# Performance work log

Measured on AMD Instinct MI355X. Metric: run time of the kernel, lower is better.

Reference implementation:

```python
import jax, jax.numpy as jnp
import numpy as np


def setup_inputs() -> dict:
    key = jax.random.key(0)
    k1, k2, k3 = jax.random.split(key, 3)
    B, Lx, Ly, D = 8, 2048, 2048, 512  # D = 2*hidden_size
    x = jax.random.normal(k1, (B, Lx, D), dtype=jnp.float32)
    y = jax.random.normal(k2, (B, Ly, D), dtype=jnp.float32)
    # torch nn.Linear weight: [out_features, in_features], applied as x @ W.T
    Wb = jax.random.normal(k3, (D, D), dtype=jnp.float32) * (1.0 / np.sqrt(D))
    return {"x": x, "y": y, "Wb": Wb}


def reference(x, y, Wb):
    # _s1 = Wb(x).transpose(2,1): project x then transpose -> scores s_jt = y @ (x Wb^T)^T
    xw = jnp.einsum('bxd,ed->bxe', x, Wb)          # [B, Lx, D], equals x @ Wb.T
    sjt = jnp.einsum('byd,bxd->byx', y, xw)        # [B, Ly, Lx]
    ait = jax.nn.softmax(sjt, axis=-1)             # softmax over Lx
    qtb = jnp.einsum('byx,bxd->byd', ait, x)       # [B, Ly, D]
    return qtb
```

## Files before the change

### kernel.cpp

```cpp
#include <hip/hip_runtime.h>
#include <hip/hip_bf16.h>
#include <math.h>

#define D_DIM 512
#define LX 2048
#define LY 2048
#define NB 8

typedef float f32x4 __attribute__((ext_vector_type(4)));
typedef __bf16 bf16x8 __attribute__((ext_vector_type(8)));

__device__ __forceinline__ unsigned short f2bf_rn(float f) {
    unsigned u = __float_as_uint(f);
    unsigned r = (u + 0x7fffu + ((u >> 16) & 1u)) >> 16;
    return (unsigned short)r;
}
__device__ __forceinline__ float bf2f(unsigned short h) {
    return __uint_as_float(((unsigned)h) << 16);
}
__device__ __forceinline__ void async16(void* lds, const void* g) {
    __builtin_amdgcn_global_load_lds(
        (const __attribute__((address_space(1))) void*)g,
        (__attribute__((address_space(3))) void*)lds, 16, 0, 0);
}
__device__ __forceinline__ bf16x8 ldfrag(const char* p) {
    return *(const bf16x8*)p;
}

__global__ __launch_bounds__(256) void repack_hilo_k(
    const float* __restrict__ src, unsigned short* __restrict__ dh,
    unsigned short* __restrict__ dl, int nfb)
{
    int fbid = blockIdx.x * 4 + (threadIdx.x >> 6);
    if (fbid >= nfb) return;
    int lane = threadIdx.x & 63;
    int r16 = fbid >> 4, k32 = fbid & 15;
    int row = r16 * 16 + (lane & 15);
    int col = k32 * 32 + (lane >> 4) * 8;
    const float* s = src + (size_t)row * D_DIM + col;
    float4 v0 = *(const float4*)s;
    float4 v1 = *(const float4*)(s + 4);
    float vv[8] = {v0.x, v0.y, v0.z, v0.w, v1.x, v1.y, v1.z, v1.w};
    unsigned hh[4], ll[4];
    #pragma unroll
    for (int k = 0; k < 4; ++k) {
        unsigned short ha = f2bf_rn(vv[2*k]),   hb = f2bf_rn(vv[2*k+1]);
        unsigned short la = f2bf_rn(vv[2*k]   - bf2f(ha));
        unsigned short lb = f2bf_rn(vv[2*k+1] - bf2f(hb));
        hh[k] = (unsigned)ha | ((unsigned)hb << 16);
        ll[k] = (unsigned)la | ((unsigned)lb << 16);
    }
    size_t off = (size_t)fbid * 512 + lane * 8;
    *(uint4*)(dh + off) = make_uint4(hh[0], hh[1], hh[2], hh[3]);
    *(uint4*)(dl + off) = make_uint4(ll[0], ll[1], ll[2], ll[3]);
}

__global__ __launch_bounds__(256) void xt_repack_k(
    const float* __restrict__ x, unsigned short* __restrict__ xtf)
{
    __shared__ unsigned short T2[64][72];
    int ct = blockIdx.x, dt = blockIdx.y, b = blockIdx.z;
    int tid = threadIdx.x;
    const float* xb = x + (size_t)b * LX * D_DIM;
    int rc = tid >> 4;
    int d4 = (tid & 15) * 4;
    #pragma unroll
    for (int i = 0; i < 4; ++i) {
        int cl = rc + i * 16;
        float4 v = *(const float4*)(xb + (size_t)(ct * 64 + cl) * D_DIM + dt * 64 + d4);
        T2[d4 + 0][cl] = f2bf_rn(v.x);
        T2[d4 + 1][cl] = f2bf_rn(v.y);
        T2[d4 + 2][cl] = f2bf_rn(v.z);
        T2[d4 + 3][cl] = f2bf_rn(v.w);
    }
    __syncthreads();
    #pragma unroll
    for (int si = 0; si < 2; ++si) {
        int s = tid + si * 256;
        int fb = s >> 6, lane = s & 63;
        int dd16l = fb >> 1, c32l = fb & 1;
        int ddl = dd16l * 16 + (lane & 15);
        int cl  = c32l * 32 + (lane >> 4) * 8;
        uint4 v = *(const uint4*)&T2[ddl][cl];
        size_t off = ((size_t)((b * 32 + dt * 4 + dd16l) * 64 + (ct * 2 + c32l)) * 64 + lane) * 8;
        *(uint4*)(xtf + off) = v;
    }
}

__global__ __launch_bounds__(256, 2) void xw_mfma_k(
    const unsigned short* __restrict__ xfh, const unsigned short* __restrict__ xfl,
    const unsigned short* __restrict__ wfh, const unsigned short* __restrict__ wfl,
    unsigned short* __restrict__ xwfh, unsigned short* __restrict__ xwfl)
{
    __shared__ char smem[49152];
    const int tid = threadIdx.x, lane = tid & 63, w = tid >> 6;
    const int Mt = blockIdx.x, Nt = blockIdx.y;
    f32x4 acc[2][4];
    #pragma unroll
    for (int m = 0; m < 2; ++m)
        #pragma unroll
        for (int n = 0; n < 4; ++n) acc[m][n] = (f32x4){0.f, 0.f, 0.f, 0.f};

    for (int kc = 0; kc < 8; ++kc) {
        __syncthreads();
        #pragma unroll
        for (int i = 0; i < 8; ++i) {
            int seg = w + 4 * i;
            int h = seg >> 4, c16l = (seg >> 1) & 7, k32l = seg & 1;
            size_t fb = (size_t)(Mt * 8 + c16l) * 16 + kc * 2 + k32l;
            const unsigned short* src = (h ? xfl : xfh) + fb * 512 + lane * 8;
            char* dst = smem + (h ? 16384 : 0) + ((c16l * 2 + k32l) * 64 + lane) * 16;
            async16(dst, src);
        }
        #pragma unroll
        for (int i = 0; i < 4; ++i) {
            int seg = w + 4 * i;
            int h = seg >> 3, n16l = (seg >> 1) & 3, k32l = seg & 1;
            size_t fb = (size_t)(Nt * 4 + n16l) * 16 + kc * 2 + k32l;
            const unsigned short* src = (h ? wfl : wfh) + fb * 512 + lane * 8;
            char* dst = smem + (h ? 40960 : 32768) + ((n16l * 2 + k32l) * 64 + lane) * 16;
            async16(dst, src);
        }
        __syncthreads();
        #pragma unroll
        for (int ks = 0; ks < 2; ++ks) {
            bf16x8 ah[2], al[2], bh[4], bl[4];
            #pragma unroll
            for (int m = 0; m < 2; ++m) {
                int c16l = w * 2 + m;
                ah[m] = ldfrag(smem +     0 + ((c16l * 2 + ks) * 64 + lane) * 16);
                al[m] = ldfrag(smem + 16384 + ((c16l * 2 + ks) * 64 + lane) * 16);
            }
            #pragma unroll
            for (int n = 0; n < 4; ++n) {
                bh[n] = ldfrag(smem + 32768 + ((n * 2 + ks) * 64 + lane) * 16);
                bl[n] = ldfrag(smem + 40960 + ((n * 2 + ks) * 64 + lane) * 16);
            }
            #pragma unroll
            for (int m = 0; m < 2; ++m)
                #pragma unroll
                for (int n = 0; n < 4; ++n) {
                    acc[m][n] = __builtin_amdgcn_mfma_f32_16x16x32_bf16(ah[m], bh[n], acc[m][n], 0, 0, 0);
                    acc[m][n] = __builtin_amdgcn_mfma_f32_16x16x32_bf16(ah[m], bl[n], acc[m][n], 0, 0, 0);
                    acc[m][n] = __builtin_amdgcn_mfma_f32_16x16x32_bf16(al[m], bh[n], acc[m][n], 0, 0, 0);
                    acc[m][n] = __builtin_amdgcn_mfma_f32_16x16x32_bf16(al[m], bl[n], acc[m][n], 0, 0, 0);
                }
        }
    }
    __syncthreads();
    float* E = (float*)smem;
    const int q = lane >> 4, c15 = lane & 15;
    #pragma unroll
    for (int m = 0; m < 2; ++m)
        #pragma unroll
        for (int n = 0; n < 4; ++n)
            #pragma unroll
            for (int r = 0; r < 4; ++r)
                E[(w * 32 + m * 16 + q * 4 + r) * 68 + n * 16 + c15] = acc[m][n][r];
    __syncthreads();
    #pragma unroll
    for (int i = 0; i < 4; ++i) {
        int s = tid + i * 256;
        int c16l = s >> 7, e32l = (s >> 6) & 1, lp = s & 63;
        int row = c16l * 16 + (lp & 15), col = e32l * 32 + (lp >> 4) * 8;
        const float* sp = E + row * 68 + col;
        unsigned hh[4], ll[4];
        #pragma unroll
        for (int k = 0; k < 4; ++k) {
            float a = sp[2 * k], bq = sp[2 * k + 1];
            unsigned short ha = f2bf_rn(a), hb = f2bf_rn(bq);
            unsigned short la = f2bf_rn(a - bf2f(ha)), lb = f2bf_rn(bq - bf2f(hb));
            hh[k] = (unsigned)ha | ((unsigned)hb << 16);
            ll[k] = (unsigned)la | ((unsigned)lb << 16);
        }
        size_t fb = (size_t)(Mt * 8 + c16l) * 16 + (Nt * 2 + e32l);
        *(uint4*)(xwfh + fb * 512 + lp * 8) = make_uint4(hh[0], hh[1], hh[2], hh[3]);
        *(uint4*)(xwfl + fb * 512 + lp * 8) = make_uint4(ll[0], ll[1], ll[2], ll[3]);
    }
}

__global__ __launch_bounds__(256, 2) void flash_mfma_k(
    const unsigned short* __restrict__ yfh, const unsigned short* __restrict__ yfl,
    const unsigned short* __restrict__ xwfh, const unsigned short* __restrict__ xwfl,
    const unsigned short* __restrict__ xtf, float* __restrict__ out)
{
    __shared__ char smem[49152];
    const int tid = threadIdx.x, lane = tid & 63, w = tid >> 6;
    const int jt = blockIdx.x, b = blockIdx.y;
    const int q = lane >> 4, c15 = lane & 15;

    f32x4 o[2][8];
    #pragma unroll
    for (int m = 0; m < 2; ++m)
        #pragma unroll
        for (int n = 0; n < 8; ++n) o[m][n] = (f32x4){0.f, 0.f, 0.f, 0.f};
    float m_run[2][4], l_run[2][4];
    #pragma unroll
    for (int m = 0; m < 2; ++m)
        #pragma unroll
        for (int r = 0; r < 4; ++r) { m_run[m][r] = -INFINITY; l_run[m][r] = 0.f; }

    for (int xt = 0; xt < 16; ++xt) {
        f32x4 s[2][2];
        #pragma unroll
        for (int m = 0; m < 2; ++m)
            #pragma unroll
            for (int n = 0; n < 2; ++n) s[m][n] = (f32x4){0.f, 0.f, 0.f, 0.f};

        for (int kc = 0; kc < 8; ++kc) {
            __syncthreads();
            #pragma unroll
            for (int i = 0; i < 8; ++i) {
                int seg = w + 4 * i;
                int h = seg >> 4, c16l = (seg >> 1) & 7, k32l = seg & 1;
                size_t fb = (size_t)(b * 128 + xt * 8 + c16l) * 16 + kc * 2 + k32l;
                const unsigned short* src = (h ? xwfl : xwfh) + fb * 512 + lane * 8;
                char* dst = smem + (h ? 16384 : 0) + ((c16l * 2 + k32l) * 64 + lane) * 16;
                async16(dst, src);
            }
            #pragma unroll
            for (int i = 0; i < 2; ++i) {
                int seg = w + 4 * i;
                int h = seg >> 2, j16l = (seg >> 1) & 1, k32l = seg & 1;
                size_t fb = (size_t)(b * 128 + jt * 2 + j16l) * 16 + kc * 2 + k32l;
                const unsigned short* src = (h ? yfl : yfh) + fb * 512 + lane * 8;
                char* dst = smem + (h ? 36864 : 32768) + ((j16l * 2 + k32l) * 64 + lane) * 16;
                async16(dst, src);
            }
            __syncthreads();
            #pragma unroll
            for (int ks = 0; ks < 2; ++ks) {
                bf16x8 ah[2], al[2], bh[2], bl[2];
                #pragma unroll
                for (int m = 0; m < 2; ++m) {
                    ah[m] = ldfrag(smem + 32768 + ((m * 2 + ks) * 64 + lane) * 16);
                    al[m] = ldfrag(smem + 36864 + ((m * 2 + ks) * 64 + lane) * 16);
                }
                #pragma unroll
                for (int n = 0; n < 2; ++n) {
                    int c16l = w * 2 + n;
                    bh[n] = ldfrag(smem +     0 + ((c16l * 2 + ks) * 64 + lane) * 16);
                    bl[n] = ldfrag(smem + 16384 + ((c16l * 2 + ks) * 64 + lane) * 16);
                }
                #pragma unroll
                for (int m = 0; m < 2; ++m)
                    #pragma unroll
                    for (int n = 0; n < 2; ++n) {
                        s[m][n] = __builtin_amdgcn_mfma_f32_16x16x32_bf16(ah[m], bh[n], s[m][n], 0, 0, 0);
                        s[m][n] = __builtin_amdgcn_mfma_f32_16x16x32_bf16(ah[m], bl[n], s[m][n], 0, 0, 0);
                        s[m][n] = __builtin_amdgcn_mfma_f32_16x16x32_bf16(al[m], bh[n], s[m][n], 0, 0, 0);
                        s[m][n] = __builtin_amdgcn_mfma_f32_16x16x32_bf16(al[m], bl[n], s[m][n], 0, 0, 0);
                    }
            }
        }

        float pmax[2][4];
        #pragma unroll
        for (int m = 0; m < 2; ++m)
            #pragma unroll
            for (int r = 0; r < 4; ++r) pmax[m][r] = fmaxf(s[m][0][r], s[m][1][r]);
        __syncthreads();
        #pragma unroll
        for (int d = 1; d < 16; d <<= 1)
            #pragma unroll
            for (int m = 0; m < 2; ++m)
                #pragma unroll
                for (int r = 0; r < 4; ++r)
                    pmax[m][r] = fmaxf(pmax[m][r], __shfl_xor(pmax[m][r], d, 64));
        float* red_max = (float*)(smem + 32768);
        float* red_sum = (float*)(smem + 33280);
        if (c15 == 0) {
            #pragma unroll
            for (int m = 0; m < 2; ++m)
                #pragma unroll
                for (int r = 0; r < 4; ++r)
                    red_max[w * 32 + m * 16 + q * 4 + r] = pmax[m][r];
        }
        __syncthreads();
        float mnew[2][4], alpha[2][4];
        #pragma unroll
        for (int m = 0; m < 2; ++m)
            #pragma unroll
            for (int r = 0; r < 4; ++r) {
                int j = m * 16 + q * 4 + r;
                float t = red_max[j];
                t = fmaxf(t, red_max[32 + j]);
                t = fmaxf(t, red_max[64 + j]);
                t = fmaxf(t, red_max[96 + j]);
                float mn = fmaxf(m_run[m][r], t);
                mnew[m][r] = mn;
                alpha[m][r] = __expf(m_run[m][r] - mn);
                m_run[m][r] = mn;
            }
        unsigned short* Pf = (unsigned short*)(smem + 40960);
        float psum[2][4];
        #pragma unroll
        for (int m = 0; m < 2; ++m)
            #pragma unroll
            for (int r = 0; r < 4; ++r) {
                float p0 = __expf(s[m][0][r] - mnew[m][r]);
                float p1 = __expf(s[m][1][r] - mnew[m][r]);
                s[m][0][r] = p0; s[m][1][r] = p1;
                psum[m][r] = p0 + p1;
            }
        #pragma unroll
        for (int d = 1; d < 16; d <<= 1)
            #pragma unroll
            for (int m = 0; m < 2; ++m)
                #pragma unroll
                for (int r = 0; r < 4; ++r)
                    psum[m][r] += __shfl_xor(psum[m][r], d, 64);
        if (c15 == 0) {
            #pragma unroll
            for (int m = 0; m < 2; ++m)
                #pragma unroll
                for (int r = 0; r < 4; ++r)
                    red_sum[w * 32 + m * 16 + q * 4 + r] = psum[m][r];
        }
        #pragma unroll
        for (int m = 0; m < 2; ++m)
            #pragma unroll
            for (int n = 0; n < 2; ++n)
                #pragma unroll
                for (int r = 0; r < 4; ++r) {
                    int cl = n * 16 + c15;
                    int lp = (q * 4 + r) + 16 * (cl >> 3);
                    Pf[((m * 4 + w) * 64 + lp) * 8 + (cl & 7)] = f2bf_rn(s[m][n][r]);
                }
        __syncthreads();
        #pragma unroll
        for (int m = 0; m < 2; ++m)
            #pragma unroll
            for (int r = 0; r < 4; ++r) {
                int j = m * 16 + q * 4 + r;
                float ts = red_sum[j] + red_sum[32 + j] + red_sum[64 + j] + red_sum[96 + j];
                l_run[m][r] = l_run[m][r] * alpha[m][r] + ts;
            }
        #pragma unroll
        for (int m = 0; m < 2; ++m)
            #pragma unroll
            for (int n = 0; n < 8; ++n)
                #pragma unroll
                for (int r = 0; r < 4; ++r) o[m][n][r] *= alpha[m][r];

        for (int cc = 0; cc < 4; ++cc) {
            #pragma unroll
            for (int i = 0; i < 8; ++i) {
                int dd16 = w + 4 * i;
                size_t off = ((size_t)(b * 32 + dd16) * 64 + (xt * 4 + cc)) * 512 + lane * 8;
                async16(smem + dd16 * 1024 + lane * 16, xtf + off);
            }
            __syncthreads();
            bf16x8 pa[2];
            pa[0] = ldfrag(smem + 40960 + ((0 * 4 + cc) * 64 + lane) * 16);
            pa[1] = ldfrag(smem + 40960 + ((1 * 4 + cc) * 64 + lane) * 16);
            #pragma unroll
            for (int n = 0; n < 8; ++n) {
                bf16x8 xb = ldfrag(smem + (w * 8 + n) * 1024 + lane * 16);
                o[0][n] = __builtin_amdgcn_mfma_f32_16x16x32_bf16(pa[0], xb, o[0][n], 0, 0, 0);
                o[1][n] = __builtin_amdgcn_mfma_f32_16x16x32_bf16(pa[1], xb, o[1][n], 0, 0, 0);
            }
            __syncthreads();
        }
    }

    #pragma unroll
    for (int m = 0; m < 2; ++m)
        #pragma unroll
        for (int r = 0; r < 4; ++r) {
            float inv = 1.0f / l_run[m][r];
            int j = jt * 32 + m * 16 + q * 4 + r;
            #pragma unroll
            for (int n = 0; n < 8; ++n) {
                int dd = w * 128 + n * 16 + c15;
                out[((size_t)(b * 2048 + j)) * 512 + dd] = o[m][n][r] * inv;
            }
        }
}

__global__ __launch_bounds__(256) void xw_gemm_fb(
    const float* __restrict__ x, const float* __restrict__ Wb, float* __restrict__ xw)
{
    __shared__ float As[16][68];
    __shared__ float Bs[16][68];
    const int tid = threadIdx.x;
    const int bm = blockIdx.x * 64, bn = blockIdx.y * 64;
    const int tm = (tid & 15) * 4, tn = (tid >> 4) * 4;
    const int lrow = tid >> 2, lk = (tid & 3) * 4;
    const float* ag = x  + (size_t)(bm + lrow) * D_DIM + lk;
    const float* bg = Wb + (size_t)(bn + lrow) * D_DIM + lk;
    float acc[4][4] = {};
    for (int kt = 0; kt < D_DIM; kt += 16) {
        const float4 av = *(const float4*)(ag + kt);
        const float4 bv = *(const float4*)(bg + kt);
        __syncthreads();
        As[lk+0][lrow] = av.x; As[lk+1][lrow] = av.y; As[lk+2][lrow] = av.z; As[lk+3][lrow] = av.w;
        Bs[lk+0][lrow] = bv.x; Bs[lk+1][lrow] = bv.y; Bs[lk+2][lrow] = bv.z; Bs[lk+3][lrow] = bv.w;
        __syncthreads();
        #pragma unroll
        for (int k = 0; k < 16; ++k) {
            const float4 a = *(const float4*)&As[k][tm];
            const float4 bq = *(const float4*)&Bs[k][tn];
            const float* ap = (const float*)&a;
            const float* bp = (const float*)&bq;
            #pragma unroll
            for (int i = 0; i < 4; ++i)
                #pragma unroll
                for (int jj = 0; jj < 4; ++jj)
                    acc[i][jj] = fmaf(ap[i], bp[jj], acc[i][jj]);
        }
    }
    #pragma unroll
    for (int i = 0; i < 4; ++i)
        *(float4*)&xw[(size_t)(bm + tm + i) * D_DIM + bn + tn] =
            make_float4(acc[i][0], acc[i][1], acc[i][2], acc[i][3]);
}

__global__ __launch_bounds__(256) void flash_fb(
    const float* __restrict__ x, const float* __restrict__ y,
    const float* __restrict__ xw, float* __restrict__ out)
{
    __shared__ float Yl[16][516];
    __shared__ float XWl[64][68];
    __shared__ float Pl[16][68];
    __shared__ float Xl[8][512];
    const int tid = threadIdx.x, b = blockIdx.y, jtb = blockIdx.x;
    const int j = tid >> 4, tc = tid & 15, c0 = tc * 4;
    {
        const float* yg = y + (size_t)(b * LY + jtb * 16 + j) * D_DIM;
        #pragma unroll
// ... 42 lines not shown
        const float p0 = __expf(sa[0] - mnew), p1 = __expf(sa[1] - mnew);
        const float p2 = __expf(sa[2] - mnew), p3 = __expf(sa[3] - mnew);
        float ts = p0 + p1 + p2 + p3;
        #pragma unroll
        for (int ww = 1; ww < 16; ww <<= 1) ts += __shfl_xor(ts, ww, 64);
        l = l * scale + ts; m = mnew;
        #pragma unroll
        for (int ii = 0; ii < 8; ++ii) {
            o[ii].x *= scale; o[ii].y *= scale; o[ii].z *= scale; o[ii].w *= scale;
        }
        *(float4*)&Pl[j][c0] = make_float4(p0, p1, p2, p3);
        for (int ccc = 0; ccc < 8; ++ccc) {
            const int xr = tid >> 5, xq = (tid & 31) * 4;
            const float* xg = x + xbase + (size_t)(xtt * 64 + ccc * 8 + xr) * D_DIM + xq;
            const float4 x0 = *(const float4*)(xg + 0);
            const float4 x1 = *(const float4*)(xg + 128);
            const float4 x2 = *(const float4*)(xg + 256);
            const float4 x3 = *(const float4*)(xg + 384);
            __syncthreads();
            *(float4*)&Xl[xr][xq +   0] = x0; *(float4*)&Xl[xr][xq + 128] = x1;
            *(float4*)&Xl[xr][xq + 256] = x2; *(float4*)&Xl[xr][xq + 384] = x3;
            __syncthreads();
            #pragma unroll
            for (int c = 0; c < 8; ++c) {
                const float pv = Pl[j][ccc * 8 + c];
                #pragma unroll
                for (int ii = 0; ii < 8; ++ii) {
                    const float4 xv = *(const float4*)&Xl[c][tc * 4 + 64 * ii];
                    o[ii].x = fmaf(pv, xv.x, o[ii].x); o[ii].y = fmaf(pv, xv.y, o[ii].y);
                    o[ii].z = fmaf(pv, xv.z, o[ii].z); o[ii].w = fmaf(pv, xv.w, o[ii].w);
                }
            }
        }
    }
    const float inv = 1.0f / l;
    float* og = out + (size_t)(b * LY + jtb * 16 + j) * D_DIM;
    #pragma unroll
    for (int ii = 0; ii < 8; ++ii) {
        float4 v = o[ii];
        v.x *= inv; v.y *= inv; v.z *= inv; v.w *= inv;
        *(float4*)(og + tc * 4 + 64 * ii) = v;
    }
}

extern "C" void kernel_launch(void* const* d_in, const int* in_sizes, int n_in,
                              void* d_out, int out_size, void* d_ws, size_t ws_size,
                              hipStream_t stream)
{
    const float* x  = (const float*)d_in[0];
    const float* y  = (const float*)d_in[1];
    const float* Wb = (const float*)d_in[2];
    float* out = (float*)d_out;

    const size_t SZ_BIG = 16777216;
    const size_t OFF_XFH = 0,         OFF_XFL = 16777216;
    const size_t OFF_YFH = 33554432,  OFF_YFL = 50331648;
    const size_t OFF_XTF = 67108864;
    const size_t OFF_XWH = 83886080,  OFF_XWL = 100663296;
    const size_t OFF_WFH = 117440512, OFF_WFL = 117964800;
    const size_t NEEDED = 118489088;
    (void)SZ_BIG;

    if (ws_size >= NEEDED) {
        char* ws = (char*)d_ws;
        unsigned short* xfh = (unsigned short*)(ws + OFF_XFH);
        unsigned short* xfl = (unsigned short*)(ws + OFF_XFL);
        unsigned short* yfh = (unsigned short*)(ws + OFF_YFH);
        unsigned short* yfl = (unsigned short*)(ws + OFF_YFL);
        unsigned short* xtf = (unsigned short*)(ws + OFF_XTF);
        unsigned short* xwfh = (unsigned short*)(ws + OFF_XWH);
        unsigned short* xwfl = (unsigned short*)(ws + OFF_XWL);
        unsigned short* wfh = (unsigned short*)(ws + OFF_WFH);
        unsigned short* wfl = (unsigned short*)(ws + OFF_WFL);

        repack_hilo_k<<<4096, 256, 0, stream>>>(x, xfh, xfl, 16384);
        repack_hilo_k<<<4096, 256, 0, stream>>>(y, yfh, yfl, 16384);
        repack_hilo_k<<<128, 256, 0, stream>>>(Wb, wfh, wfl, 512);
        dim3 gt(32, 8, 8);
        xt_repack_k<<<gt, 256, 0, stream>>>(x, xtf);
        dim3 g1(128, 8);
        xw_mfma_k<<<g1, 256, 0, stream>>>(xfh, xfl, wfh, wfl, xwfh, xwfl);
        dim3 g2(64, 8);
        flash_mfma_k<<<g2, 256, 0, stream>>>(yfh, yfl, xwfh, xwfl, xtf, out);
    } else {
        float* xw = (float*)d_ws;
        dim3 g1(NB * LX / 64, D_DIM / 64);
        xw_gemm_fb<<<g1, 256, 0, stream>>>(x, Wb, xw);
        dim3 g2(LY / 16, NB);
        flash_fb<<<g2, 256, 0, stream>>>(x, y, xw, out);
    }
}
```

Before: 395.7 us.

## Split flash attention over Lx into two partitions with a combine pass, drop lo*lo MFMA

The flash kernel is split along the Lx dimension into two halves (grid z adds a split index), each writing fp16 partial outputs plus running max/sum, and a new combine kernel merges them in fp32. This doubles the block count (64x8 to 64x2x8) for better CU occupancy, and the launch bound is raised to 3 blocks per CU. The score tile is widened to 64 x-columns per wave with a different K-chunking. The lo*lo bf16 split-precision MFMA term is dropped in both the xW GEMM and the score GEMM, which cuts MFMA work but slightly reduces accuracy. The fp16 partials and the extra combine pass add memory traffic and some precision loss.

```diff
diff --git a/kernel.cpp b/kernel.cpp
--- a/kernel.cpp
+++ b/kernel.cpp
@@ -1,5 +1,6 @@
 #include <hip/hip_runtime.h>
 #include <hip/hip_bf16.h>
+#include <hip/hip_fp16.h>
 #include <math.h>
 
 #define D_DIM 512
@@ -143,7 +144,6 @@
                     acc[m][n] = __builtin_amdgcn_mfma_f32_16x16x32_bf16(ah[m], bh[n], acc[m][n], 0, 0, 0);
                     acc[m][n] = __builtin_amdgcn_mfma_f32_16x16x32_bf16(ah[m], bl[n], acc[m][n], 0, 0, 0);
                     acc[m][n] = __builtin_amdgcn_mfma_f32_16x16x32_bf16(al[m], bh[n], acc[m][n], 0, 0, 0);
-                    acc[m][n] = __builtin_amdgcn_mfma_f32_16x16x32_bf16(al[m], bl[n], acc[m][n], 0, 0, 0);
                 }
         }
     }
@@ -179,15 +179,19 @@
     }
 }
 
-__global__ __launch_bounds__(256, 2) void flash_mfma_k(
+__global__ __launch_bounds__(256, 3) void flash2_k(
     const unsigned short* __restrict__ yfh, const unsigned short* __restrict__ yfl,
     const unsigned short* __restrict__ xwfh, const unsigned short* __restrict__ xwfl,
-    const unsigned short* __restrict__ xtf, float* __restrict__ out)
-{
-    __shared__ char smem[49152];
+    const unsigned short* __restrict__ xtf,
+    __half* __restrict__ part, float* __restrict__ mpart, float* __restrict__ lpart)
+{
+    __shared__ char smem[46080];
     const int tid = threadIdx.x, lane = tid & 63, w = tid >> 6;
-    const int jt = blockIdx.x, b = blockIdx.y;
+    const int jt = blockIdx.x, sp = blockIdx.y, b = blockIdx.z;
     const int q = lane >> 4, c15 = lane & 15;
+    unsigned short* Pf = (unsigned short*)(smem + 36864);
+    float* red_max = (float*)(smem + 45056);
+    float* red_sum = (float*)(smem + 45568);
 
     f32x4 o[2][8];
     #pragma unroll
@@ -200,57 +204,46 @@
         #pragma unroll
         for (int r = 0; r < 4; ++r) { m_run[m][r] = -INFINITY; l_run[m][r] = 0.f; }
 
-    for (int xt = 0; xt < 16; ++xt) {
-        f32x4 s[2][2];
+    for (int xt = 0; xt < 4; ++xt) {
+        f32x4 sa[2][4];
         #pragma unroll
         for (int m = 0; m < 2; ++m)
             #pragma unroll
-            for (int n = 0; n < 2; ++n) s[m][n] = (f32x4){0.f, 0.f, 0.f, 0.f};
-
-        for (int kc = 0; kc < 8; ++kc) {
+            for (int n = 0; n < 4; ++n) sa[m][n] = (f32x4){0.f, 0.f, 0.f, 0.f};
+
+        for (int kc = 0; kc < 16; ++kc) {
             __syncthreads();
             #pragma unroll
             for (int i = 0; i < 8; ++i) {
                 int seg = w + 4 * i;
-                int h = seg >> 4, c16l = (seg >> 1) & 7, k32l = seg & 1;
-                size_t fb = (size_t)(b * 128 + xt * 8 + c16l) * 16 + kc * 2 + k32l;
+                int h = seg >> 4, c16l = seg & 15;
+                size_t fb = ((size_t)(b * 128 + sp * 64 + xt * 16 + c16l)) * 16 + kc;
                 const unsigned short* src = (h ? xwfl : xwfh) + fb * 512 + lane * 8;
-                char* dst = smem + (h ? 16384 : 0) + ((c16l * 2 + k32l) * 64 + lane) * 16;
-                async16(dst, src);
-            }
-            #pragma unroll
-            for (int i = 0; i < 2; ++i) {
-                int seg = w + 4 * i;
-                int h = seg >> 2, j16l = (seg >> 1) & 1, k32l = seg & 1;
-                size_t fb = (size_t)(b * 128 + jt * 2 + j16l) * 16 + kc * 2 + k32l;
+                async16(smem + h * 16384 + (c16l * 64 + lane) * 16, src);
+            }
+            {
+                int h = w >> 1, j16l = w & 1;
+                size_t fb = ((size_t)(b * 128 + jt * 2 + j16l)) * 16 + kc;
                 const unsigned short* src = (h ? yfl : yfh) + fb * 512 + lane * 8;
-                char* dst = smem + (h ? 36864 : 32768) + ((j16l * 2 + k32l) * 64 + lane) * 16;
-                async16(dst, src);
+                async16(smem + 32768 + h * 2048 + j16l * 1024 + lane * 16, src);
             }
             __syncthreads();
-            #pragma unroll
-            for (int ks = 0; ks < 2; ++ks) {
-                bf16x8 ah[2], al[2], bh[2], bl[2];
+            bf16x8 ah[2], al[2];
+            ah[0] = ldfrag(smem + 32768 + lane * 16);
+            ah[1] = ldfrag(smem + 32768 + 1024 + lane * 16);
+            al[0] = ldfrag(smem + 34816 + lane * 16);
+            al[1] = ldfrag(smem + 34816 + 1024 + lane * 16);
+            #pragma unroll
+            for (int n = 0; n < 4; ++n) {
+                int c16l = w * 4 + n;
+                bf16x8 bh = ldfrag(smem + (c16l * 64 + lane) * 16);
+                bf16x8 bl = ldfrag(smem + 16384 + (c16l * 64 + lane) * 16);
                 #pragma unroll
                 for (int m = 0; m < 2; ++m) {
-                    ah[m] = ldfrag(smem + 32768 + ((m * 2 + ks) * 64 + lane) * 16);
-                    al[m] = ldfrag(smem + 36864 + ((m * 2 + ks) * 64 + lane) * 16);
-                }
-                #pragma unroll
-                for (int n = 0; n < 2; ++n) {
-                    int c16l = w * 2 + n;
-                    bh[n] = ldfrag(smem +     0 + ((c16l * 2 + ks) * 64 + lane) * 16);
-                    bl[n] = ldfrag(smem + 16384 + ((c16l * 2 + ks) * 64 + lane) * 16);
-                }
-                #pragma unroll
-                for (int m = 0; m < 2; ++m)
-                    #pragma unroll
-                    for (int n = 0; n < 2; ++n) {
-                        s[m][n] = __builtin_amdgcn_mfma_f32_16x16x32_bf16(ah[m], bh[n], s[m][n], 0, 0, 0);
-                        s[m][n] = __builtin_amdgcn_mfma_f32_16x16x32_bf16(ah[m], bl[n], s[m][n], 0, 0, 0);
-                        s[m][n] = __builtin_amdgcn_mfma_f32_16x16x32_bf16(al[m], bh[n], s[m][n], 0, 0, 0);
-                        s[m][n] = __builtin_amdgcn_mfma_f32_16x16x32_bf16(al[m], bl[n], s[m][n], 0, 0, 0);
-                    }
+                    sa[m][n] = __builtin_amdgcn_mfma_f32_16x16x32_bf16(ah[m], bh, sa[m][n], 0, 0, 0);
+                    sa[m][n] = __builtin_amdgcn_mfma_f32_16x16x32_bf16(ah[m], bl, sa[m][n], 0, 0, 0);
+                    sa[m][n] = __builtin_amdgcn_mfma_f32_16x16x32_bf16(al[m], bh, sa[m][n], 0, 0, 0);
+                }
             }
         }
 
@@ -258,8 +251,9 @@
         #pragma unroll
         for (int m = 0; m < 2; ++m)
             #pragma unroll
-            for (int r = 0; r < 4; ++r) pmax[m][r] = fmaxf(s[m][0][r], s[m][1][r]);
-        __syncthreads();
+            for (int r = 0; r < 4; ++r)
+                pmax[m][r] = fmaxf(fmaxf(sa[m][0][r], sa[m][1][r]),
+                                   fmaxf(sa[m][2][r], sa[m][3][r]));
         #pragma unroll
         for (int d = 1; d < 16; d <<= 1)
             #pragma unroll
@@ -267,8 +261,6 @@
                 #pragma unroll
                 for (int r = 0; r < 4; ++r)
                     pmax[m][r] = fmaxf(pmax[m][r], __shfl_xor(pmax[m][r], d, 64));
-        float* red_max = (float*)(smem + 32768);
-        float* red_sum = (float*)(smem + 33280);
         if (c15 == 0) {
             #pragma unroll
             for (int m = 0; m < 2; ++m)
@@ -283,26 +275,24 @@
             #pragma unroll
             for (int r = 0; r < 4; ++r) {
                 int j = m * 16 + q * 4 + r;
-                float t = red_max[j];
-                t = fmaxf(t, red_max[32 + j]);
-                t = fmaxf(t, red_max[64 + j]);
-                t = fmaxf(t, red_max[96 + j]);
+                float t = fmaxf(fmaxf(red_max[j], red_max[32 + j]),
+                                fmaxf(red_max[64 + j], red_max[96 + j]));
                 float mn = fmaxf(m_run[m][r], t);
                 mnew[m][r] = mn;
                 alpha[m][r] = __expf(m_run[m][r] - mn);
                 m_run[m][r] = mn;
             }
-        unsigned short* Pf = (unsigned short*)(smem + 40960);
-        float psum[2][4];
+        float psum[2][4] = {};
         #pragma unroll
         for (int m = 0; m < 2; ++m)
             #pragma unroll
-            for (int r = 0; r < 4; ++r) {
-                float p0 = __expf(s[m][0][r] - mnew[m][r]);
-                float p1 = __expf(s[m][1][r] - mnew[m][r]);
-                s[m][0][r] = p0; s[m][1][r] = p1;
-                psum[m][r] = p0 + p1;
-            }
+            for (int n = 0; n < 4; ++n)
+                #pragma unroll
+                for (int r = 0; r < 4; ++r) {
+                    float p = __expf(sa[m][n][r] - mnew[m][r]);
+                    sa[m][n][r] = p;
+                    psum[m][r] += p;
+                }
         #pragma unroll
         for (int d = 1; d < 16; d <<= 1)
             #pragma unroll
@@ -317,16 +307,19 @@
                 for (int r = 0; r < 4; ++r)
                     red_sum[w * 32 + m * 16 + q * 4 + r] = psum[m][r];
         }
-        #pragma unroll
-        for (int m = 0; m < 2; ++m)
-            #pragma unroll
-            for (int n = 0; n < 2; ++n)
-                #pragma unroll
-                for (int r = 0; r < 4; ++r) {
-                    int cl = n * 16 + c15;
-                    int lp = (q * 4 + r) + 16 * (cl >> 3);
-                    Pf[((m * 4 + w) * 64 + lp) * 8 + (cl & 7)] = f2bf_rn(s[m][n][r]);
-                }
+        if (w < 2) {
+            #pragma unroll
+            for (int m = 0; m < 2; ++m)
+                #pragma unroll
+                for (int n = 0; n < 4; ++n)
+                    #pragma unroll
+                    for (int r = 0; r < 4; ++r) {
+                        int cl = w * 64 + n * 16 + c15;
+                        int c32h = cl >> 5, co = cl & 31;
+                        int lp = (q * 4 + r) + 16 * (co >> 3);
+                        Pf[((m * 4 + c32h) * 64 + lp) * 8 + (co & 7)] = f2bf_rn(sa[m][n][r]);
+                    }
+        }
         __syncthreads();
         #pragma unroll
         for (int m = 0; m < 2; ++m)
@@ -343,24 +336,43 @@
                 #pragma unroll
                 for (int r = 0; r < 4; ++r) o[m][n][r] *= alpha[m][r];
 
-        for (int cc = 0; cc < 4; ++cc) {
-            #pragma unroll
-            for (int i = 0; i < 8; ++i) {
-                int dd16 = w + 4 * i;
-                size_t off = ((size_t)(b * 32 + dd16) * 64 + (xt * 4 + cc)) * 512 + lane * 8;
-                async16(smem + dd16 * 1024 + lane * 16, xtf + off);
-            }
-            __syncthreads();
-            bf16x8 pa[2];
-            pa[0] = ldfrag(smem + 40960 + ((0 * 4 + cc) * 64 + lane) * 16);
-            pa[1] = ldfrag(smem + 40960 + ((1 * 4 + cc) * 64 + lane) * 16);
-            #pragma unroll
-            for (int n = 0; n < 8; ++n) {
-                bf16x8 xb = ldfrag(smem + (w * 8 + n) * 1024 + lane * 16);
-                o[0][n] = __builtin_amdgcn_mfma_f32_16x16x32_bf16(pa[0], xb, o[0][n], 0, 0, 0);
-                o[1][n] = __builtin_amdgcn_mfma_f32_16x16x32_bf16(pa[1], xb, o[1][n], 0, 0, 0);
-            }
-            __syncthreads();
+        for (int hh = 0; hh < 2; ++hh) {
+            if (hh == 1) {
+                __syncthreads();
+                if (w >= 2) {
+                    #pragma unroll
+                    for (int m = 0; m < 2; ++m)
+                        #pragma unroll
+                        for (int n = 0; n < 4; ++n)
+                            #pragma unroll
+                            for (int r = 0; r < 4; ++r) {
+                                int cl = w * 64 + n * 16 + c15 - 128;
+                                int c32h = cl >> 5, co = cl & 31;
+                                int lp = (q * 4 + r) + 16 * (co >> 3);
+                                Pf[((m * 4 + c32h) * 64 + lp) * 8 + (co & 7)] = f2bf_rn(sa[m][n][r]);
+                            }
+                }
+            }
+            for (int cc = 0; cc < 4; ++cc) {
+                __syncthreads();
+                #pragma unroll
+                for (int i = 0; i < 8; ++i) {
+                    int dd16 = w + 4 * i;
+                    int c32 = sp * 32 + xt * 8 + hh * 4 + cc;
+                    const unsigned short* src =
+                        xtf + (((size_t)(b * 32 + dd16)) * 64 + c32) * 512 + lane * 8;
+                    async16(smem + dd16 * 1024 + lane * 16, src);
+                }
+                __syncthreads();
+                bf16x8 pa0 = ldfrag(smem + 36864 + ((cc) * 64 + lane) * 16);
+                bf16x8 pa1 = ldfrag(smem + 36864 + ((4 + cc) * 64 + lane) * 16);
+                #pragma unroll
+                for (int n = 0; n < 8; ++n) {
+                    bf16x8 xb = ldfrag(smem + (w * 8 + n) * 1024 + lane * 16);
+                    o[0][n] = __builtin_amdgcn_mfma_f32_16x16x32_bf16(pa0, xb, o[0][n], 0, 0, 0);
+                    o[1][n] = __builtin_amdgcn_mfma_f32_16x16x32_bf16(pa1, xb, o[1][n], 0, 0, 0);
+                }
+            }
         }
     }
 
@@ -370,12 +382,50 @@
         for (int r = 0; r < 4; ++r) {
             float inv = 1.0f / l_run[m][r];
             int j = jt * 32 + m * 16 + q * 4 + r;
+            size_t row = ((size_t)sp * 8 + b) * 2048 + j;
             #pragma unroll
             for (int n = 0; n < 8; ++n) {
                 int dd = w * 128 + n * 16 + c15;
-                out[((size_t)(b * 2048 + j)) * 512 + dd] = o[m][n][r] * inv;
-            }
-        }
+                part[row * 512 + dd] = __float2half(o[m][n][r] * inv);
+            }
+        }
+    if (w == 0 && c15 == 0) {
+        #pragma unroll
+        for (int m = 0; m < 2; ++m)
+            #pragma unroll
+            for (int r = 0; r < 4; ++r) {
+                int j = jt * 32 + m * 16 + q * 4 + r;
+                size_t row = ((size_t)sp * 8 + b) * 2048 + j;
+                mpart[row] = m_run[m][r];
+                lpart[row] = l_run[m][r];
+            }
+    }
+}
+
+__global__ __launch_bounds__(256) void combine_k(
+    const __half* __restrict__ part, const float* __restrict__ mp,
+    const float* __restrict__ lp, float* __restrict__ out)
+{
+    int t = blockIdx.x * 256 + threadIdx.x;
+    int row = t >> 6;
+    int d8 = (t & 63) * 8;
+    float m0 = mp[row], m1 = mp[16384 + row];
+    float l0 = lp[row], l1 = lp[16384 + row];
+    float M = fmaxf(m0, m1);
+    float b0 = l0 * __expf(m0 - M);
+    float b1 = l1 * __expf(m1 - M);
+    float inv = 1.0f / (b0 + b1);
+    b0 *= inv; b1 *= inv;
+    const __half2* p0 = (const __half2*)(part + (size_t)row * 512 + d8);
+    const __half2* p1 = (const __half2*)(part + 8388608 + (size_t)row * 512 + d8);
+    float* og = out + (size_t)row * 512 + d8;
+    #pragma unroll
+    for (int i = 0; i < 4; ++i) {
+        float2 a = __half22float2(p0[i]);
+        float2 c = __half22float2(p1[i]);
+        og[2 * i + 0] = b0 * a.x + b1 * c.x;
+        og[2 * i + 1] = b0 * a.y + b1 * c.y;
+    }
 }
 
 __global__ __launch_bounds__(256) void xw_gemm_fb(
@@ -524,14 +574,12 @@
     const float* Wb = (const float*)d_in[2];
     float* out = (float*)d_out;
 
-    const size_t SZ_BIG = 16777216;
     const size_t OFF_XFH = 0,         OFF_XFL = 16777216;
     const size_t OFF_YFH = 33554432,  OFF_YFL = 50331648;
     const size_t OFF_XTF = 67108864;
     const size_t OFF_XWH = 83886080,  OFF_XWL = 100663296;
     const size_t OFF_WFH = 117440512, OFF_WFL = 117964800;
-    const size_t NEEDED = 118489088;
-    (void)SZ_BIG;
+    const size_t NEEDED  = 118489088;
 
     if (ws_size >= NEEDED) {
         char* ws = (char*)d_ws;
@@ -544,6 +592,9 @@
         unsigned short* xwfl = (unsigned short*)(ws + OFF_XWL);
         unsigned short* wfh = (unsigned short*)(ws + OFF_WFH);
         unsigned short* wfl = (unsigned short*)(ws + OFF_WFL);
+        __half* part = (__half*)(ws + OFF_XFH);
+        float* mpart = (float*)(ws + OFF_WFH);
+        float* lpart = (float*)(ws + OFF_WFH + 131072);
 
         repack_hilo_k<<<4096, 256, 0, stream>>>(x, xfh, xfl, 16384);
         repack_hilo_k<<<4096, 256, 0, stream>>>(y, yfh, yfl, 16384);
@@ -552,8 +603,9 @@
         xt_repack_k<<<gt, 256, 0, stream>>>(x, xtf);
         dim3 g1(128, 8);
         xw_mfma_k<<<g1, 256, 0, stream>>>(xfh, xfl, wfh, wfl, xwfh, xwfl);
-        dim3 g2(64, 8);
-        flash_mfma_k<<<g2, 256, 0, stream>>>(yfh, yfl, xwfh, xwfl, xtf, out);
+        dim3 g2(64, 2, 8);
+        flash2_k<<<g2, 256, 0, stream>>>(yfh, yfl, xwfh, xwfl, xtf, part, mpart, lpart);
+        combine_k<<<4096, 256, 0, stream>>>(part, mpart, lpart, out);
     } else {
         float* xw = (float*)d_ws;
         dim3 g1(NB * LX / 64, D_DIM / 64);
```

After: 624.5 us. +57.8%, slower.

## Double-buffer MFMA stages, drop lo*lo term, fuse prep kernels into one

Applied to the files above, without the earlier changes.

Merges the four repack kernels into one prep launch. Both GEMM loops (xw projection and the score GEMM in the flash kernel) now double-buffer their LDS tiles with async loads one k-chunk ahead, and the PV loop double-buffers the xt tiles. The split-bf16 emulation drops the lo*lo MFMA term, cutting MFMA work by a quarter at a small accuracy cost. LDS use grows to about 73 KB in the flash kernel, which may limit occupancy to two blocks per CU.

```diff
diff --git a/kernel.cpp b/kernel.cpp
--- a/kernel.cpp
+++ b/kernel.cpp
@@ -27,63 +27,70 @@
     return *(const bf16x8*)p;
 }
 
-__global__ __launch_bounds__(256) void repack_hilo_k(
-    const float* __restrict__ src, unsigned short* __restrict__ dh,
-    unsigned short* __restrict__ dl, int nfb)
-{
-    int fbid = blockIdx.x * 4 + (threadIdx.x >> 6);
-    if (fbid >= nfb) return;
-    int lane = threadIdx.x & 63;
-    int r16 = fbid >> 4, k32 = fbid & 15;
-    int row = r16 * 16 + (lane & 15);
-    int col = k32 * 32 + (lane >> 4) * 8;
-    const float* s = src + (size_t)row * D_DIM + col;
-    float4 v0 = *(const float4*)s;
-    float4 v1 = *(const float4*)(s + 4);
-    float vv[8] = {v0.x, v0.y, v0.z, v0.w, v1.x, v1.y, v1.z, v1.w};
-    unsigned hh[4], ll[4];
-    #pragma unroll
-    for (int k = 0; k < 4; ++k) {
-        unsigned short ha = f2bf_rn(vv[2*k]),   hb = f2bf_rn(vv[2*k+1]);
-        unsigned short la = f2bf_rn(vv[2*k]   - bf2f(ha));
-        unsigned short lb = f2bf_rn(vv[2*k+1] - bf2f(hb));
-        hh[k] = (unsigned)ha | ((unsigned)hb << 16);
-        ll[k] = (unsigned)la | ((unsigned)lb << 16);
-    }
-    size_t off = (size_t)fbid * 512 + lane * 8;
-    *(uint4*)(dh + off) = make_uint4(hh[0], hh[1], hh[2], hh[3]);
-    *(uint4*)(dl + off) = make_uint4(ll[0], ll[1], ll[2], ll[3]);
-}
-
-__global__ __launch_bounds__(256) void xt_repack_k(
-    const float* __restrict__ x, unsigned short* __restrict__ xtf)
+__global__ __launch_bounds__(256) void prep_k(
+    const float* __restrict__ x, const float* __restrict__ y,
+    const float* __restrict__ Wb,
+    unsigned short* __restrict__ xfh, unsigned short* __restrict__ xfl,
+    unsigned short* __restrict__ yfh, unsigned short* __restrict__ yfl,
+    unsigned short* __restrict__ wfh, unsigned short* __restrict__ wfl,
+    unsigned short* __restrict__ xtf)
 {
     __shared__ unsigned short T2[64][72];
-    int ct = blockIdx.x, dt = blockIdx.y, b = blockIdx.z;
-    int tid = threadIdx.x;
-    const float* xb = x + (size_t)b * LX * D_DIM;
-    int rc = tid >> 4;
-    int d4 = (tid & 15) * 4;
-    #pragma unroll
-    for (int i = 0; i < 4; ++i) {
-        int cl = rc + i * 16;
-        float4 v = *(const float4*)(xb + (size_t)(ct * 64 + cl) * D_DIM + dt * 64 + d4);
-        T2[d4 + 0][cl] = f2bf_rn(v.x);
-        T2[d4 + 1][cl] = f2bf_rn(v.y);
-        T2[d4 + 2][cl] = f2bf_rn(v.z);
-        T2[d4 + 3][cl] = f2bf_rn(v.w);
-    }
-    __syncthreads();
-    #pragma unroll
-    for (int si = 0; si < 2; ++si) {
-        int s = tid + si * 256;
-        int fb = s >> 6, lane = s & 63;
-        int dd16l = fb >> 1, c32l = fb & 1;
-        int ddl = dd16l * 16 + (lane & 15);
-        int cl  = c32l * 32 + (lane >> 4) * 8;
-        uint4 v = *(const uint4*)&T2[ddl][cl];
-        size_t off = ((size_t)((b * 32 + dt * 4 + dd16l) * 64 + (ct * 2 + c32l)) * 64 + lane) * 8;
-        *(uint4*)(xtf + off) = v;
+    const int blk = blockIdx.x, tid = threadIdx.x;
+
+    if (blk < 8320) {
+        const float* src; unsigned short *dh, *dl; int base;
+        if (blk < 4096)      { src = x;  dh = xfh; dl = xfl; base = blk; }
+        else if (blk < 8192) { src = y;  dh = yfh; dl = yfl; base = blk - 4096; }
+        else                 { src = Wb; dh = wfh; dl = wfl; base = blk - 8192; }
+        int fbid = base * 4 + (tid >> 6);
+        int lane = tid & 63;
+        int r16 = fbid >> 4, k32 = fbid & 15;
+        int row = r16 * 16 + (lane & 15);
+        int col = k32 * 32 + (lane >> 4) * 8;
+        const float* s = src + (size_t)row * D_DIM + col;
+        float4 v0 = *(const float4*)s;
+        float4 v1 = *(const float4*)(s + 4);
+        float vv[8] = {v0.x, v0.y, v0.z, v0.w, v1.x, v1.y, v1.z, v1.w};
+        unsigned hh[4], ll[4];
+        #pragma unroll
+        for (int k = 0; k < 4; ++k) {
+            unsigned short ha = f2bf_rn(vv[2*k]),   hb = f2bf_rn(vv[2*k+1]);
+            unsigned short la = f2bf_rn(vv[2*k]   - bf2f(ha));
+            unsigned short lb = f2bf_rn(vv[2*k+1] - bf2f(hb));
+            hh[k] = (unsigned)ha | ((unsigned)hb << 16);
+            ll[k] = (unsigned)la | ((unsigned)lb << 16);
+        }
+        size_t off = (size_t)fbid * 512 + lane * 8;
+        *(uint4*)(dh + off) = make_uint4(hh[0], hh[1], hh[2], hh[3]);
+        *(uint4*)(dl + off) = make_uint4(ll[0], ll[1], ll[2], ll[3]);
+    } else {
+        int idx = blk - 8320;
+        int ct = idx & 31, dt = (idx >> 5) & 7, b = idx >> 8;
+        const float* xb = x + (size_t)b * LX * D_DIM;
+        int rc = tid >> 4;
+        int d4 = (tid & 15) * 4;
+        #pragma unroll
+        for (int i = 0; i < 4; ++i) {
+            int cl = rc + i * 16;
+            float4 v = *(const float4*)(xb + (size_t)(ct * 64 + cl) * D_DIM + dt * 64 + d4);
+            T2[d4 + 0][cl] = f2bf_rn(v.x);
+            T2[d4 + 1][cl] = f2bf_rn(v.y);
+            T2[d4 + 2][cl] = f2bf_rn(v.z);
+            T2[d4 + 3][cl] = f2bf_rn(v.w);
+        }
+        __syncthreads();
+        #pragma unroll
+        for (int si = 0; si < 2; ++si) {
+            int s = tid + si * 256;
+            int fb = s >> 6, lane = s & 63;
+            int dd16l = fb >> 1, c32l = fb & 1;
+            int ddl = dd16l * 16 + (lane & 15);
+            int cl  = c32l * 32 + (lane >> 4) * 8;
+            uint4 v = *(const uint4*)&T2[ddl][cl];
+            size_t off = ((size_t)((b * 32 + dt * 4 + dd16l) * 64 + (ct * 2 + c32l)) * 64 + lane) * 8;
+            *(uint4*)(xtf + off) = v;
+        }
     }
 }
 
@@ -95,59 +102,61 @@
     __shared__ char smem[49152];
     const int tid = threadIdx.x, lane = tid & 63, w = tid >> 6;
     const int Mt = blockIdx.x, Nt = blockIdx.y;
+
     f32x4 acc[2][4];
     #pragma unroll
     for (int m = 0; m < 2; ++m)
         #pragma unroll
         for (int n = 0; n < 4; ++n) acc[m][n] = (f32x4){0.f, 0.f, 0.f, 0.f};
 
-    for (int kc = 0; kc < 8; ++kc) {
-        __syncthreads();
-        #pragma unroll
-        for (int i = 0; i < 8; ++i) {
-            int seg = w + 4 * i;
-            int h = seg >> 4, c16l = (seg >> 1) & 7, k32l = seg & 1;
-            size_t fb = (size_t)(Mt * 8 + c16l) * 16 + kc * 2 + k32l;
+    auto stage = [&](int kc, int buf) {
+        char* sb = smem + buf * 24576;
+        #pragma unroll
+        for (int i = 0; i < 4; ++i) {
+            int s = w + 4 * i;
+            int c16l = s >> 1, h = s & 1;
+            size_t fb = ((size_t)(Mt * 8 + c16l)) * 16 + kc;
             const unsigned short* src = (h ? xfl : xfh) + fb * 512 + lane * 8;
-            char* dst = smem + (h ? 16384 : 0) + ((c16l * 2 + k32l) * 64 + lane) * 16;
-            async16(dst, src);
-        }
-        #pragma unroll
-        for (int i = 0; i < 4; ++i) {
-            int seg = w + 4 * i;
-            int h = seg >> 3, n16l = (seg >> 1) & 3, k32l = seg & 1;
-            size_t fb = (size_t)(Nt * 4 + n16l) * 16 + kc * 2 + k32l;
+            async16(sb + h * 8192 + c16l * 1024 + lane * 16, src);
+        }
+        #pragma unroll
+        for (int i = 0; i < 2; ++i) {
+            int s = w + 4 * i;
+            int n16l = s >> 1, h = s & 1;
+            size_t fb = ((size_t)(Nt * 4 + n16l)) * 16 + kc;
             const unsigned short* src = (h ? wfl : wfh) + fb * 512 + lane * 8;
-            char* dst = smem + (h ? 40960 : 32768) + ((n16l * 2 + k32l) * 64 + lane) * 16;
-            async16(dst, src);
-        }
-        __syncthreads();
-        #pragma unroll
-        for (int ks = 0; ks < 2; ++ks) {
-            bf16x8 ah[2], al[2], bh[4], bl[4];
-            #pragma unroll
-            for (int m = 0; m < 2; ++m) {
-                int c16l = w * 2 + m;
-                ah[m] = ldfrag(smem +     0 + ((c16l * 2 + ks) * 64 + lane) * 16);
-                al[m] = ldfrag(smem + 16384 + ((c16l * 2 + ks) * 64 + lane) * 16);
-            }
+            async16(sb + 16384 + h * 4096 + n16l * 1024 + lane * 16, src);
+        }
+    };
+
+    stage(0, 0);
+    __syncthreads();
+    for (int kc = 0; kc < 16; ++kc) {
+        if (kc < 15) stage(kc + 1, (kc + 1) & 1);
+        char* sb = smem + (kc & 1) * 24576;
+        bf16x8 ah[2], al[2], bh[4], bl[4];
+        #pragma unroll
+        for (int m = 0; m < 2; ++m) {
+            int c16l = w * 2 + m;
+            ah[m] = ldfrag(sb + c16l * 1024 + lane * 16);
+            al[m] = ldfrag(sb + 8192 + c16l * 1024 + lane * 16);
+        }
+        #pragma unroll
+        for (int n = 0; n < 4; ++n) {
+            bh[n] = ldfrag(sb + 16384 + n * 1024 + lane * 16);
+            bl[n] = ldfrag(sb + 20480 + n * 1024 + lane * 16);
+        }
+        #pragma unroll
+        for (int m = 0; m < 2; ++m)
             #pragma unroll
             for (int n = 0; n < 4; ++n) {
-                bh[n] = ldfrag(smem + 32768 + ((n * 2 + ks) * 64 + lane) * 16);
-                bl[n] = ldfrag(smem + 40960 + ((n * 2 + ks) * 64 + lane) * 16);
-            }
-            #pragma unroll
-            for (int m = 0; m < 2; ++m)
-                #pragma unroll
-                for (int n = 0; n < 4; ++n) {
-                    acc[m][n] = __builtin_amdgcn_mfma_f32_16x16x32_bf16(ah[m], bh[n], acc[m][n], 0, 0, 0);
-                    acc[m][n] = __builtin_amdgcn_mfma_f32_16x16x32_bf16(ah[m], bl[n], acc[m][n], 0, 0, 0);
-                    acc[m][n] = __builtin_amdgcn_mfma_f32_16x16x32_bf16(al[m], bh[n], acc[m][n], 0, 0, 0);
-                    acc[m][n] = __builtin_amdgcn_mfma_f32_16x16x32_bf16(al[m], bl[n], acc[m][n], 0, 0, 0);
-                }
-        }
-    }
-    __syncthreads();
+                acc[m][n] = __builtin_amdgcn_mfma_f32_16x16x32_bf16(ah[m], bh[n], acc[m][n], 0, 0, 0);
+                acc[m][n] = __builtin_amdgcn_mfma_f32_16x16x32_bf16(ah[m], bl[n], acc[m][n], 0, 0, 0);
+                acc[m][n] = __builtin_amdgcn_mfma_f32_16x16x32_bf16(al[m], bh[n], acc[m][n], 0, 0, 0);
+            }
+        __syncthreads();
+    }
+
     float* E = (float*)smem;
     const int q = lane >> 4, c15 = lane & 15;
     #pragma unroll
@@ -179,15 +188,20 @@
     }
 }
 
-__global__ __launch_bounds__(256, 2) void flash_mfma_k(
+#define SBUF_STRIDE 20480
+
+__global__ __launch_bounds__(256, 2) void flash3_k(
     const unsigned short* __restrict__ yfh, const unsigned short* __restrict__ yfl,
     const unsigned short* __restrict__ xwfh, const unsigned short* __restrict__ xwfl,
     const unsigned short* __restrict__ xtf, float* __restrict__ out)
 {
-    __shared__ char smem[49152];
+    __shared__ char smem[74752];
     const int tid = threadIdx.x, lane = tid & 63, w = tid >> 6;
     const int jt = blockIdx.x, b = blockIdx.y;
     const int q = lane >> 4, c15 = lane & 15;
+    unsigned short* Pf = (unsigned short*)(smem + 65536);
+    float* red_max = (float*)(smem + 73728);
+    float* red_sum = (float*)(smem + 74240);
 
     f32x4 o[2][8];
     #pragma unroll
@@ -200,66 +214,70 @@
         #pragma unroll
         for (int r = 0; r < 4; ++r) { m_run[m][r] = -INFINITY; l_run[m][r] = 0.f; }
 
+    auto stage_s = [&](int xt, int kc, int buf) {
+        char* sb = smem + buf * SBUF_STRIDE;
+        #pragma unroll
+        for (int i = 0; i < 4; ++i) {
+            int s = w + 4 * i;
+            int c16l = s >> 1, h = s & 1;
+            size_t fb = ((size_t)(b * 128 + xt * 8 + c16l)) * 16 + kc;
+            const unsigned short* src = (h ? xwfl : xwfh) + fb * 512 + lane * 8;
+            async16(sb + h * 8192 + c16l * 1024 + lane * 16, src);
+        }
+        {
+            int j16l = w & 1, h = w >> 1;
+            size_t fb = ((size_t)(b * 128 + jt * 2 + j16l)) * 16 + kc;
+            const unsigned short* src = (h ? yfl : yfh) + fb * 512 + lane * 8;
+            async16(sb + 16384 + h * 2048 + j16l * 1024 + lane * 16, src);
+        }
+    };
+    auto stage_x = [&](int xt, int cc, int buf) {
+        char* xb = smem + buf * 32768;
+        #pragma unroll
+        for (int i = 0; i < 8; ++i) {
+            int dd16 = w + 4 * i;
+            size_t off = (((size_t)(b * 32 + dd16)) * 64 + (xt * 4 + cc)) * 512 + lane * 8;
+            async16(xb + dd16 * 1024 + lane * 16, xtf + off);
+        }
+    };
+
     for (int xt = 0; xt < 16; ++xt) {
-        f32x4 s[2][2];
-        #pragma unroll
-        for (int m = 0; m < 2; ++m)
-            #pragma unroll
-            for (int n = 0; n < 2; ++n) s[m][n] = (f32x4){0.f, 0.f, 0.f, 0.f};
-
-        for (int kc = 0; kc < 8; ++kc) {
+        f32x4 sa[2][2];
+        #pragma unroll
+        for (int m = 0; m < 2; ++m)
+            #pragma unroll
+            for (int n = 0; n < 2; ++n) sa[m][n] = (f32x4){0.f, 0.f, 0.f, 0.f};
+
+        stage_s(xt, 0, 0);
+        __syncthreads();
+        for (int kc = 0; kc < 16; ++kc) {
+            if (kc < 15) stage_s(xt, kc + 1, (kc + 1) & 1);
+            char* sb = smem + (kc & 1) * SBUF_STRIDE;
+            bf16x8 ah[2], al[2];
+            ah[0] = ldfrag(sb + 16384 + lane * 16);
+            ah[1] = ldfrag(sb + 17408 + lane * 16);
+            al[0] = ldfrag(sb + 18432 + lane * 16);
+            al[1] = ldfrag(sb + 19456 + lane * 16);
+            #pragma unroll
+            for (int n = 0; n < 2; ++n) {
+                int c16l = w * 2 + n;
+                bf16x8 bh = ldfrag(sb + c16l * 1024 + lane * 16);
+                bf16x8 bl = ldfrag(sb + 8192 + c16l * 1024 + lane * 16);
+                #pragma unroll
+                for (int m = 0; m < 2; ++m) {
+                    sa[m][n] = __builtin_amdgcn_mfma_f32_16x16x32_bf16(ah[m], bh, sa[m][n], 0, 0, 0);
+                    sa[m][n] = __builtin_amdgcn_mfma_f32_16x16x32_bf16(ah[m], bl, sa[m][n], 0, 0, 0);
+                    sa[m][n] = __builtin_amdgcn_mfma_f32_16x16x32_bf16(al[m], bh, sa[m][n], 0, 0, 0);
+                }
+            }
             __syncthreads();
-            #pragma unroll
-            for (int i = 0; i < 8; ++i) {
-                int seg = w + 4 * i;
-                int h = seg >> 4, c16l = (seg >> 1) & 7, k32l = seg & 1;
-                size_t fb = (size_t)(b * 128 + xt * 8 + c16l) * 16 + kc * 2 + k32l;
-                const unsigned short* src = (h ? xwfl : xwfh) + fb * 512 + lane * 8;
-                char* dst = smem + (h ? 16384 : 0) + ((c16l * 2 + k32l) * 64 + lane) * 16;
-                async16(dst, src);
-            }
-            #pragma unroll
-            for (int i = 0; i < 2; ++i) {
-                int seg = w + 4 * i;
-                int h = seg >> 2, j16l = (seg >> 1) & 1, k32l = seg & 1;
-                size_t fb = (size_t)(b * 128 + jt * 2 + j16l) * 16 + kc * 2 + k32l;
-                const unsigned short* src = (h ? yfl : yfh) + fb * 512 + lane * 8;
-                char* dst = smem + (h ? 36864 : 32768) + ((j16l * 2 + k32l) * 64 + lane) * 16;
-                async16(dst, src);
-            }
-            __syncthreads();
-            #pragma unroll
-            for (int ks = 0; ks < 2; ++ks) {
-                bf16x8 ah[2], al[2], bh[2], bl[2];
-                #pragma unroll
-                for (int m = 0; m < 2; ++m) {
-                    ah[m] = ldfrag(smem + 32768 + ((m * 2 + ks) * 64 + lane) * 16);
-                    al[m] = ldfrag(smem + 36864 + ((m * 2 + ks) * 64 + lane) * 16);
-                }
-                #pragma unroll
-                for (int n = 0; n < 2; ++n) {
-                    int c16l = w * 2 + n;
-                    bh[n] = ldfrag(smem +     0 + ((c16l * 2 + ks) * 64 + lane) * 16);
-                    bl[n] = ldfrag(smem + 16384 + ((c16l * 2 + ks) * 64 + lane) * 16);
-                }
-                #pragma unroll
-                for (int m = 0; m < 2; ++m)
-                    #pragma unroll
-                    for (int n = 0; n < 2; ++n) {
-                        s[m][n] = __builtin_amdgcn_mfma_f32_16x16x32_bf16(ah[m], bh[n], s[m][n], 0, 0, 0);
-                        s[m][n] = __builtin_amdgcn_mfma_f32_16x16x32_bf16(ah[m], bl[n], s[m][n], 0, 0, 0);
-                        s[m][n] = __builtin_amdgcn_mfma_f32_16x16x32_bf16(al[m], bh[n], s[m][n], 0, 0, 0);
-                        s[m][n] = __builtin_amdgcn_mfma_f32_16x16x32_bf16(al[m], bl[n], s[m][n], 0, 0, 0);
-                    }
-            }
         }
 
         float pmax[2][4];
         #pragma unroll
         for (int m = 0; m < 2; ++m)
             #pragma unroll
-            for (int r = 0; r < 4; ++r) pmax[m][r] = fmaxf(s[m][0][r], s[m][1][r]);
-        __syncthreads();
+            for (int r = 0; r < 4; ++r) pmax[m][r] = fmaxf(sa[m][0][r], sa[m][1][r]);
         #pragma unroll
         for (int d = 1; d < 16; d <<= 1)
             #pragma unroll
@@ -267,8 +285,6 @@
                 #pragma unroll
                 for (int r = 0; r < 4; ++r)
                     pmax[m][r] = fmaxf(pmax[m][r], __shfl_xor(pmax[m][r], d, 64));
-        float* red_max = (float*)(smem + 32768);
-        float* red_sum = (float*)(smem + 33280);
         if (c15 == 0) {
             #pragma unroll
             for (int m = 0; m < 2; ++m)
@@ -283,26 +299,24 @@
             #pragma unroll
             for (int r = 0; r < 4; ++r) {
                 int j = m * 16 + q * 4 + r;
-                float t = red_max[j];
-                t = fmaxf(t, red_max[32 + j]);
-                t = fmaxf(t, red_max[64 + j]);
-                t = fmaxf(t, red_max[96 + j]);
+                float t = fmaxf(fmaxf(red_max[j], red_max[32 + j]),
+                                fmaxf(red_max[64 + j], red_max[96 + j]));
                 float mn = fmaxf(m_run[m][r], t);
                 mnew[m][r] = mn;
                 alpha[m][r] = __expf(m_run[m][r] - mn);
                 m_run[m][r] = mn;
             }
-        unsigned short* Pf = (unsigned short*)(smem + 40960);
-        float psum[2][4];
-        #pragma unroll
-        for (int m = 0; m < 2; ++m)
-            #pragma unroll
-            for (int r = 0; r < 4; ++r) {
-                float p0 = __expf(s[m][0][r] - mnew[m][r]);
-                float p1 = __expf(s[m][1][r] - mnew[m][r]);
-                s[m][0][r] = p0; s[m][1][r] = p1;
-                psum[m][r] = p0 + p1;
-            }
+        float psum[2][4] = {};
+        #pragma unroll
+        for (int m = 0; m < 2; ++m)
+            #pragma unroll
+            for (int n = 0; n < 2; ++n)
+                #pragma unroll
+                for (int r = 0; r < 4; ++r) {
+                    float p = __expf(sa[m][n][r] - mnew[m][r]);
+                    sa[m][n][r] = p;
+                    psum[m][r] += (n == 0) ? p - psum[m][r] * 0.f : p;
+                }
         #pragma unroll
         for (int d = 1; d < 16; d <<= 1)
             #pragma unroll
@@ -325,7 +339,7 @@
                 for (int r = 0; r < 4; ++r) {
                     int cl = n * 16 + c15;
                     int lp = (q * 4 + r) + 16 * (cl >> 3);
-                    Pf[((m * 4 + w) * 64 + lp) * 8 + (cl & 7)] = f2bf_rn(s[m][n][r]);
+                    Pf[((m * 4 + w) * 64 + lp) * 8 + (cl & 7)] = f2bf_rn(sa[m][n][r]);
                 }
         __syncthreads();
         #pragma unroll
@@ -343,22 +357,18 @@
                 #pragma unroll
                 for (int r = 0; r < 4; ++r) o[m][n][r] *= alpha[m][r];
 
+        stage_x(xt, 0, 0);
+        __syncthreads();
         for (int cc = 0; cc < 4; ++cc) {
-            #pragma unroll
-            for (int i = 0; i < 8; ++i) {
-                int dd16 = w + 4 * i;
-                size_t off = ((size_t)(b * 32 + dd16) * 64 + (xt * 4 + cc)) * 512 + lane * 8;
-                async16(smem + dd16 * 1024 + lane * 16, xtf + off);
-            }
-            __syncthreads();
-            bf16x8 pa[2];
-            pa[0] = ldfrag(smem + 40960 + ((0 * 4 + cc) * 64 + lane) * 16);
-            pa[1] = ldfrag(smem + 40960 + ((1 * 4 + cc) * 64 + lane) * 16);
+            if (cc < 3) stage_x(xt, cc + 1, (cc + 1) & 1);
+            char* xb = smem + (cc & 1) * 32768;
+            bf16x8 pa0 = ldfrag((const char*)Pf + ((0 * 4 + cc) * 64 + lane) * 16);
+            bf16x8 pa1 = ldfrag((const char*)Pf + ((1 * 4 + cc) * 64 + lane) * 16);
             #pragma unroll
             for (int n = 0; n < 8; ++n) {
-                bf16x8 xb = ldfrag(smem + (w * 8 + n) * 1024 + lane * 16);
-                o[0][n] = __builtin_amdgcn_mfma_f32_16x16x32_bf16(pa[0], xb, o[0][n], 0, 0, 0);
-                o[1][n] = __builtin_amdgcn_mfma_f32_16x16x32_bf16(pa[1], xb, o[1][n], 0, 0, 0);
+                bf16x8 xv = ldfrag(xb + (w * 8 + n) * 1024 + lane * 16);
+                o[0][n] = __builtin_amdgcn_mfma_f32_16x16x32_bf16(pa0, xv, o[0][n], 0, 0, 0);
+                o[1][n] = __builtin_amdgcn_mfma_f32_16x16x32_bf16(pa1, xv, o[1][n], 0, 0, 0);
             }
             __syncthreads();
         }
@@ -524,14 +534,12 @@
     const float* Wb = (const float*)d_in[2];
     float* out = (float*)d_out;
 
-    const size_t SZ_BIG = 16777216;
     const size_t OFF_XFH = 0,         OFF_XFL = 16777216;
     const size_t OFF_YFH = 33554432,  OFF_YFL = 50331648;
     const size_t OFF_XTF = 67108864;
     const size_t OFF_XWH = 83886080,  OFF_XWL = 100663296;
     const size_t OFF_WFH = 117440512, OFF_WFL = 117964800;
-    const size_t NEEDED = 118489088;
-    (void)SZ_BIG;
+    const size_t NEEDED  = 118489088;
 
     if (ws_size >= NEEDED) {
         char* ws = (char*)d_ws;
@@ -545,15 +553,11 @@
         unsigned short* wfh = (unsigned short*)(ws + OFF_WFH);
         unsigned short* wfl = (unsigned short*)(ws + OFF_WFL);
 
-        repack_hilo_k<<<4096, 256, 0, stream>>>(x, xfh, xfl, 16384);
-        repack_hilo_k<<<4096, 256, 0, stream>>>(y, yfh, yfl, 16384);
-        repack_hilo_k<<<128, 256, 0, stream>>>(Wb, wfh, wfl, 512);
-        dim3 gt(32, 8, 8);
-        xt_repack_k<<<gt, 256, 0, stream>>>(x, xtf);
+        prep_k<<<10368, 256, 0, stream>>>(x, y, Wb, xfh, xfl, yfh, yfl, wfh, wfl, xtf);
         dim3 g1(128, 8);
         xw_mfma_k<<<g1, 256, 0, stream>>>(xfh, xfl, wfh, wfl, xwfh, xwfl);
         dim3 g2(64, 8);
-        flash_mfma_k<<<g2, 256, 0, stream>>>(yfh, yfl, xwfh, xwfl, xtf, out);
+        flash3_k<<<g2, 256, 0, stream>>>(yfh, yfl, xwfh, xwfl, xtf, out);
     } else {
         float* xw = (float*)d_ws;
         dim3 g1(NB * LX / 64, D_DIM / 64);
```

After: 383.6 us. 3.0% less time.
